# Optimization experiments

Measured on AMD Instinct MI355X. Metric: run time of the kernel, lower is better.

## Reference

```python
import jax, jax.numpy as jnp
import numpy as np


def setup_inputs() -> dict:
    key = jax.random.key(0)
    k1, k2, k3 = jax.random.split(key, 3)
    B, S, D = 2, 2048, 4096
    x = jax.random.normal(k1, (B, S, D), dtype=jnp.float32)
    weight = jax.random.normal(k2, (D, D), dtype=jnp.float32)  # [out, in]
    bias = jax.random.normal(k3, (D,), dtype=jnp.float32)
    return {"x": x, "weight": weight, "bias": bias}


def reference(x, weight, bias):
    # STE binarization: forward uses sign(W) (sign(0)=0, matching torch.sign)
    w = jnp.sign(weight)
    # F.linear: x @ w.T + b
    return jnp.einsum('bsk,nk->bsn', x, w) + bias
```

## Files before the change

### kernel.cpp

```cpp
#include <hip/hip_runtime.h>
#include <hip/hip_bf16.h>
#include <stdint.h>

#define M_DIM 4096
#define N_DIM 4096
#define K_DIM 4096
#define NTO 64

typedef float f32x4 __attribute__((ext_vector_type(4)));
typedef __bf16 bf16x8 __attribute__((ext_vector_type(8)));
typedef float f4 __attribute__((ext_vector_type(4)));
typedef unsigned int u32x4 __attribute__((ext_vector_type(4)));
typedef unsigned short u16x8 __attribute__((ext_vector_type(8)));

__device__ __forceinline__ uint16_t f32_to_bf16_rn(float f) {
  uint32_t u = __float_as_uint(f);
  u += 0x7fffu + ((u >> 16) & 1u);
  return (uint16_t)(u >> 16);
}

__global__ void convert_fused(const u32x4* __restrict__ w4,
                              u16x8* __restrict__ s8,
                              const f4* __restrict__ x4,
                              uint16_t* __restrict__ Ab, int n8) {
  const int half = 2048;
  if (blockIdx.x < half) {
    int idx = blockIdx.x * 256 + threadIdx.x;
    int stride = half * 256;
    for (int i = idx; i < n8; i += stride) {
      u32x4 a = w4[2 * i], b = w4[2 * i + 1];
      u16x8 o;
#pragma unroll
      for (int j = 0; j < 4; ++j) {
        uint32_t ua = a[j], ub = b[j];
        o[j] = ((ua & 0x7fffffffu) == 0u)
                   ? (uint16_t)0
                   : (uint16_t)(0x3F80u | ((ua >> 16) & 0x8000u));
        o[4 + j] = ((ub & 0x7fffffffu) == 0u)
                       ? (uint16_t)0
                       : (uint16_t)(0x3F80u | ((ub >> 16) & 0x8000u));
      }
      s8[i] = o;
    }
  } else {
    int idx = (blockIdx.x - half) * 256 + threadIdx.x;
    int stride = half * 256;
    for (int i = idx; i < n8; i += stride) {
      f4 a = x4[2 * i], b = x4[2 * i + 1];
      u16x8 h, l;
#pragma unroll
      for (int j = 0; j < 4; ++j) {
        uint16_t hb = f32_to_bf16_rn(a[j]);
        h[j] = hb;
        l[j] = f32_to_bf16_rn(a[j] - __uint_as_float((uint32_t)hb << 16));
        uint16_t hb2 = f32_to_bf16_rn(b[j]);
        h[4 + j] = hb2;
        l[4 + j] = f32_to_bf16_rn(b[j] - __uint_as_float((uint32_t)hb2 << 16));
      }
      int flat = i * 8;
      int m = flat >> 12;
      int k = flat & 4095;
      *(u16x8*)&Ab[(size_t)m * 8192 + k] = h;
      *(u16x8*)&Ab[(size_t)m * 8192 + 4096 + k] = l;
    }
  }
}

__device__ __forceinline__ void gload_lds16(const void* g, void* l) {
  __builtin_amdgcn_global_load_lds(
      (__attribute__((address_space(1))) void*)(g),
      (__attribute__((address_space(3))) void*)(l),
      16, 0, 0);
}

__global__ __launch_bounds__(512, 2)
void bingemm8(const uint16_t* __restrict__ Ab, const uint16_t* __restrict__ Bs,
              const float* __restrict__ bias, float* __restrict__ out) {
  __shared__ uint16_t sAh[2][8192];
  __shared__ uint16_t sAl[2][8192];
  __shared__ uint16_t sB[2][2][8192];

  const int t = threadIdx.x;
  const int lane = t & 63;
  const int w = t >> 6;
  const int r15 = lane & 15;

  const int bid = blockIdx.x;
  const int swz = (bid & 7) * 32 + (bid >> 3);
  const int bm = (swz >> 4) * 256;
  const int bn = (swz & 15) * 256;

  const int srow = t >> 3;
  const int scol = (((t & 7) ^ (srow & 7)) * 8);
  const size_t aThr = (size_t)(bm + srow) * 8192 + scol;
  const size_t bThr = (size_t)(bn + srow) * 4096 + scol;

#define STAGE_AH(KT, HH)                                            \
  do {                                                              \
    const uint16_t* g = Ab + aThr + (size_t)(HH) * 128 * 8192 +     \
                        (size_t)(KT) * 64;                          \
    gload_lds16(g, &sAh[HH][t * 8]);                                \
    gload_lds16(g + (size_t)64 * 8192, &sAh[HH][t * 8 + 4096]);     \
  } while (0)
#define STAGE_AL(KT, HH)                                            \
  do {                                                              \
    const uint16_t* g = Ab + aThr + (size_t)(HH) * 128 * 8192 +     \
                        4096 + (size_t)(KT) * 64;                   \
    gload_lds16(g, &sAl[HH][t * 8]);                                \
    gload_lds16(g + (size_t)64 * 8192, &sAl[HH][t * 8 + 4096]);     \
  } while (0)
#define STAGE_B(KT, HH, BUF)                                        \
  do {                                                              \
    const uint16_t* g = Bs + bThr + (size_t)(HH) * 128 * 4096 +     \
                        (size_t)(KT) * 64;                          \
    gload_lds16(g, &sB[BUF][HH][t * 8]);                            \
    gload_lds16(g + (size_t)64 * 4096, &sB[BUF][HH][t * 8 + 4096]); \
  } while (0)

  const int klane = lane >> 4;
  const int cb0 = (klane * 16) ^ ((lane & 7) << 4);
  const int whA = w >> 2;
  const int whB = (w & 3) >> 1;
  const int wcl = (w & 1) * 64;
  const int eA0 = r15 * 64 + (cb0 >> 1);
  const int eA1 = eA0 ^ 32;
  const int eB0 = (wcl + r15) * 64 + (cb0 >> 1);
  const int eB1 = eB0 ^ 32;

  bf16x8 rAa[4], rAb[4], rBa[4], rBb[4];
  f32x4 acc[8][4];
#pragma unroll
  for (int m = 0; m < 8; ++m)
#pragma unroll
    for (int n = 0; n < 4; ++n) acc[m][n] = (f32x4){0.f, 0.f, 0.f, 0.f};

#define LOAD_A0(SRC, MOFF)                                                  \
  {                                                                         \
    _Pragma("unroll") for (int m = 0; m < 4; ++m)                           \
        rAa[m] = *(const bf16x8*)&SRC[whA][eA0 + ((MOFF) + m) * 1024];      \
  }
#define LOAD_A1(SRC, MOFF)                                                  \
  {                                                                         \
    _Pragma("unroll") for (int m = 0; m < 4; ++m)                           \
        rAb[m] = *(const bf16x8*)&SRC[whA][eA1 + ((MOFF) + m) * 1024];      \
  }
#define LOAD_B0(BUF)                                                        \
  {                                                                         \
    _Pragma("unroll") for (int n = 0; n < 4; ++n)                           \
        rBa[n] = *(const bf16x8*)&sB[BUF][whB][eB0 + n * 1024];             \
  }
#define LOAD_B1(BUF)                                                        \
  {                                                                         \
    _Pragma("unroll") for (int n = 0; n < 4; ++n)                           \
        rBb[n] = *(const bf16x8*)&sB[BUF][whB][eB1 + n * 1024];             \
  }
#define MFMA32(MB)                                                          \
  {                                                                         \
    _Pragma("unroll") for (int mm = 0; mm < 4; ++mm)                        \
    _Pragma("unroll") for (int nn = 0; nn < 4; ++nn) {                      \
      acc[(MB) + mm][nn] = __builtin_amdgcn_mfma_f32_16x16x32_bf16(         \
          rAa[mm], rBa[nn], acc[(MB) + mm][nn], 0, 0, 0);                   \
      acc[(MB) + mm][nn] = __builtin_amdgcn_mfma_f32_16x16x32_bf16(         \
          rAb[mm], rBb[nn], acc[(MB) + mm][nn], 0, 0, 0);                   \
    }                                                                       \
  }
#define PH_PRE()                                        \
  __builtin_amdgcn_s_barrier();                         \
  asm volatile("s_waitcnt lgkmcnt(0)" ::: "memory");    \
  __builtin_amdgcn_sched_barrier(0);                    \
  __builtin_amdgcn_s_setprio(1);
#define PH_POST()                                       \
  __builtin_amdgcn_s_setprio(0);                        \
  __builtin_amdgcn_s_barrier();
#define PH_POST_VM4()                                   \
  __builtin_amdgcn_s_setprio(0);                        \
  asm volatile("s_waitcnt vmcnt(4)" ::: "memory");      \
  __builtin_amdgcn_s_barrier();
#define PH_POST_VM0()                                   \
  __builtin_amdgcn_s_setprio(0);                        \
  asm volatile("s_waitcnt vmcnt(0)" ::: "memory");      \
  __builtin_amdgcn_s_barrier();

#define TILE_BODY(KT)                                           \
  {                                                             \
    const int b = (KT) & 1;                                     \
    const int bn1 = b ^ 1;                                      \
    const int kp1 = ((KT) + 1 < NTO) ? ((KT) + 1) : (NTO - 1);  \
                                  \
    LOAD_A0(sAh, 0);                                            \
    LOAD_A1(sAh, 0);                                            \
    LOAD_B0(b);                                                 \
    LOAD_B1(b);                                                 \
    STAGE_AL(KT, 0);                                            \
    STAGE_AL(KT, 1);                                            \
    PH_PRE();                                                   \
    MFMA32(0);                                                  \
    PH_POST();                                                  \
                                           \
    LOAD_A0(sAh, 4);                                            \
    LOAD_A1(sAh, 4);                                            \
    STAGE_B(kp1, 0, bn1);                                       \
    STAGE_B(kp1, 1, bn1);                                       \
    PH_PRE();                                                   \
    MFMA32(4);                                                  \
    PH_POST_VM4();                                              \
                           \
    LOAD_A0(sAl, 0);                                            \
    LOAD_A1(sAl, 0);                                            \
    STAGE_AH(kp1, 0);                                           \
    STAGE_AH(kp1, 1);                                           \
    PH_PRE();                                                   \
    MFMA32(0);                                                  \
    PH_POST();                                                  \
                                           \
    LOAD_A0(sAl, 4);                                            \
    LOAD_A1(sAl, 4);                                            \
    PH_PRE();                                                   \
    MFMA32(4);                                                  \
    PH_POST_VM0();                                              \
  }

  STAGE_AH(0, 0);
  STAGE_AH(0, 1);
  STAGE_B(0, 0, 0);
  STAGE_B(0, 1, 0);
  asm volatile("s_waitcnt vmcnt(0)" ::: "memory");
  __builtin_amdgcn_s_barrier();

  for (int i2 = 0; i2 < NTO / 2; ++i2) {
    TILE_BODY(2 * i2);
    TILE_BODY(2 * i2 + 1);
  }

  asm volatile("s_waitcnt vmcnt(0)" ::: "memory");

  const int rowg = (lane >> 4) * 4;
#pragma unroll
  for (int n = 0; n < 4; ++n) {
    const int col = bn + (w & 3) * 64 + n * 16 + r15;
    const float bv = bias[col];
#pragma unroll
    for (int m = 0; m < 8; ++m) {
      const int row0 = bm + (w >> 2) * 128 + m * 16 + rowg;
#pragma unroll
      for (int k = 0; k < 4; ++k)
        out[(size_t)(row0 + k) * N_DIM + col] = acc[m][n][k] + bv;
    }
  }
}

__global__ void fallback_gemm(const float* __restrict__ x,
                              const float* __restrict__ w,
                              const float* __restrict__ bias,
                              float* __restrict__ out) {
  __shared__ float sx[16][17];
  __shared__ float sw[16][17];
  int tx = threadIdx.x & 15, ty = threadIdx.x >> 4;
  int m = blockIdx.y * 16 + ty;
  int n = blockIdx.x * 16 + tx;
  float acc = 0.f;
  for (int k0 = 0; k0 < K_DIM; k0 += 16) {
    sx[ty][tx] = x[(size_t)m * K_DIM + k0 + tx];
    float wv = w[(size_t)(blockIdx.x * 16 + ty) * K_DIM + k0 + tx];
    sw[ty][tx] = (wv > 0.f) ? 1.f : ((wv < 0.f) ? -1.f : 0.f);
    __syncthreads();
#pragma unroll
    for (int kk = 0; kk < 16; ++kk) acc += sx[ty][kk] * sw[tx][kk];
    __syncthreads();
  }
  out[(size_t)m * N_DIM + n] = acc + bias[n];
}

extern "C" void kernel_launch(void* const* d_in, const int* in_sizes, int n_in,
                              void* d_out, int out_size, void* d_ws,
                              size_t ws_size, hipStream_t stream) {
  const float* x = (const float*)d_in[0];
  const float* w = (const float*)d_in[1];
  const float* bias = (const float*)d_in[2];
  float* out = (float*)d_out;

  const size_t elems = (size_t)N_DIM * K_DIM;
  const size_t need = elems * 2u * 3u;

  if (ws_size < need) {
    dim3 grid(N_DIM / 16, M_DIM / 16);
    fallback_gemm<<<grid, 256, 0, stream>>>(x, w, bias, out);
    return;
  }

  uint16_t* Sb = (uint16_t*)d_ws;
  uint16_t* Ab = Sb + elems;

  const int n8 = (int)(elems / 8);
  convert_fused<<<4096, 256, 0, stream>>>((const u32x4*)w, (u16x8*)Sb,
                                          (const f4*)x, Ab, n8);

  bingemm8<<<dim3(256), 512, 0, stream>>>(Ab, Sb, bias, out);
}
```

Before: 378.6 us.

## Cut per-tile barriers from eight to two and issue global stages earlier

Replaces the barrier pairs around each of the four MFMA phases with only two workgroup barriers per K tile, placed after the vmcnt waits. Global-to-LDS staging for the current tile's A-low half and the next tile's B is now issued at the start of the tile, before the LDS reads. The goal is to reduce barrier stalls and give the global loads longer to overlap with MFMA work. In exchange it loosens the ordering between LDS writes and reads and depends on the buffer lifetimes still keeping the reads race-free.

```diff
diff --git a/kernel.cpp b/kernel.cpp
--- a/kernel.cpp
+++ b/kernel.cpp
@@ -164,60 +164,49 @@
           rAb[mm], rBb[nn], acc[(MB) + mm][nn], 0, 0, 0);                   \
     }                                                                       \
   }
-#define PH_PRE()                                        \
-  __builtin_amdgcn_s_barrier();                         \
+#define WAITK()                                         \
   asm volatile("s_waitcnt lgkmcnt(0)" ::: "memory");    \
-  __builtin_amdgcn_sched_barrier(0);                    \
-  __builtin_amdgcn_s_setprio(1);
-#define PH_POST()                                       \
-  __builtin_amdgcn_s_setprio(0);                        \
-  __builtin_amdgcn_s_barrier();
-#define PH_POST_VM4()                                   \
-  __builtin_amdgcn_s_setprio(0);                        \
-  asm volatile("s_waitcnt vmcnt(4)" ::: "memory");      \
-  __builtin_amdgcn_s_barrier();
-#define PH_POST_VM0()                                   \
-  __builtin_amdgcn_s_setprio(0);                        \
-  asm volatile("s_waitcnt vmcnt(0)" ::: "memory");      \
-  __builtin_amdgcn_s_barrier();
+  __builtin_amdgcn_sched_barrier(0);
+#define MFMA_SEG(MB)                                    \
+  __builtin_amdgcn_s_setprio(1);                        \
+  MFMA32(MB);                                           \
+  __builtin_amdgcn_s_setprio(0);
 
 #define TILE_BODY(KT)                                           \
   {                                                             \
     const int b = (KT) & 1;                                     \
     const int bn1 = b ^ 1;                                      \
     const int kp1 = ((KT) + 1 < NTO) ? ((KT) + 1) : (NTO - 1);  \
-                                  \
+                                      \
+    STAGE_AL(KT, 0);                                            \
+    STAGE_AL(KT, 1);                                            \
+    STAGE_B(kp1, 0, bn1);                                       \
+    STAGE_B(kp1, 1, bn1);                                       \
     LOAD_A0(sAh, 0);                                            \
     LOAD_A1(sAh, 0);                                            \
     LOAD_B0(b);                                                 \
     LOAD_B1(b);                                                 \
-    STAGE_AL(KT, 0);                                            \
-    STAGE_AL(KT, 1);                                            \
-    PH_PRE();                                                   \
-    MFMA32(0);                                                  \
-    PH_POST();                                                  \
-                                           \
+    WAITK();                                                    \
+    MFMA_SEG(0);                                                \
     LOAD_A0(sAh, 4);                                            \
     LOAD_A1(sAh, 4);                                            \
-    STAGE_B(kp1, 0, bn1);                                       \
-    STAGE_B(kp1, 1, bn1);                                       \
-    PH_PRE();                                                   \
-    MFMA32(4);                                                  \
-    PH_POST_VM4();                                              \
-                           \
+    WAITK();                                                    \
+    MFMA_SEG(4);                                                \
+    asm volatile("s_waitcnt vmcnt(4)" ::: "memory");            \
+    __builtin_amdgcn_s_barrier();                               \
+                      \
+    STAGE_AH(kp1, 0);                                           \
+    STAGE_AH(kp1, 1);                                           \
     LOAD_A0(sAl, 0);                                            \
     LOAD_A1(sAl, 0);                                            \
-    STAGE_AH(kp1, 0);                                           \
-    STAGE_AH(kp1, 1);                                           \
-    PH_PRE();                                                   \
-    MFMA32(0);                                                  \
-    PH_POST();                                                  \
-                                           \
+    WAITK();                                                    \
+    MFMA_SEG(0);                                                \
     LOAD_A0(sAl, 4);                                            \
     LOAD_A1(sAl, 4);                                            \
-    PH_PRE();                                                   \
-    MFMA32(4);                                                  \
-    PH_POST_VM0();                                              \
+    WAITK();                                                    \
+    MFMA_SEG(4);                                                \
+    asm volatile("s_waitcnt vmcnt(0)" ::: "memory");            \
+    __builtin_amdgcn_s_barrier();                               \
   }
 
   STAGE_AH(0, 0);
```

Measured after the change: 370.7 us. 2.1% less time.
